# Kernel optimization log

Hardware: AMD Instinct MI355X
Metric: run time of the kernel (lower is better)

Reference implementation:

```python
import jax, jax.numpy as jnp
import numpy as np

B, S, H, E, D, K = 2, 4096, 1024, 8, 2048, 2


def setup_inputs() -> dict:
    key = jax.random.key(0)
    ks = jax.random.split(key, 6)
    scale = 0.02
    return {
        "x": jax.random.normal(ks[0], (B, S, H), dtype=jnp.float32),
        "gate_w": jax.random.normal(ks[1], (E, H), dtype=jnp.float32) * scale,
        "w1": jax.random.normal(ks[2], (E, H, D), dtype=jnp.float32) * scale,
        "b1": jnp.zeros((E, D), dtype=jnp.float32),
        "w2": jax.random.normal(ks[3], (E, D, H), dtype=jnp.float32) * scale,
        "b2": jnp.zeros((E, H), dtype=jnp.float32),
    }


def reference(x, gate_w, w1, b1, w2, b2):
    b, s, h = x.shape
    e = gate_w.shape[0]
    # Router
    router_logits = jnp.einsum('bsh,eh->bse', x, gate_w)
    router_probs = jax.nn.softmax(router_logits, axis=-1)
    top_k_probs, expert_idx = jax.lax.top_k(router_probs, K)      # [B,S,K]
    top_k_probs = top_k_probs / top_k_probs.sum(axis=-1, keepdims=True)
    # Aux load-balancing loss (faithful to source: mean over batch only -> [S,E])
    oh = jax.nn.one_hot(expert_idx, e, dtype=x.dtype)             # [B,S,K,E]
    tokens_per_expert = oh.sum(axis=-2).mean(axis=0)              # [S,E]
    avg_prob = router_probs.mean(axis=(0, 1))                     # [E]
    aux_loss = e * (tokens_per_expert * avg_prob).sum()
    # Dense combine weights per token per expert: [B*S, E]
    combine = (oh * top_k_probs[..., None]).sum(axis=-2).reshape(-1, e)
    # Expert MLPs, batched over experts (grouped GEMM form)
    xf = x.reshape(-1, h)                                         # [T,H]
    hid = jax.nn.gelu(jnp.einsum('th,ehd->etd', xf, w1) + b1[:, None, :],
                      approximate=False)                          # [E,T,D]
    y = jnp.einsum('etd,edh->eth', hid, w2) + b2[:, None, :]      # [E,T,H]
    out = jnp.einsum('te,eth->th', combine, y)                    # [T,H]
    return out.reshape(b, s, h), aux_loss
```

## Files before the change

kernel.cpp:

```cpp
#include <hip/hip_runtime.h>
#include <hip/hip_bf16.h>
#include <math.h>

#define Bdim 2
#define Sdim 4096
#define Hdim 1024
#define Edim 8
#define Ddim 2048
#define Tdim (Bdim*Sdim)

typedef __attribute__((ext_vector_type(8))) __bf16 bfv8;
typedef __attribute__((ext_vector_type(8))) short s16x8;
typedef __attribute__((ext_vector_type(4))) short s16x4;
typedef __attribute__((ext_vector_type(4))) float f32x4;

__device__ __forceinline__ short f2bf(float f) {
    union { float f; unsigned u; } a; a.f = f;
    unsigned r = (a.u + 0x7fffu + ((a.u >> 16) & 1u)) >> 16;
    return (short)r;
}
__device__ __forceinline__ float bf2f(short s) {
    union { unsigned u; float f; } a; a.u = ((unsigned)(unsigned short)s) << 16;
    return a.f;
}
__device__ __forceinline__ float fgelu(float x) {
    float u = fminf(x * (1.5957691f + 0.07135481f * x * x), 60.0f);
    float t = __expf(u);
    return x * t / (t + 1.0f);
}

typedef const __attribute__((address_space(1))) unsigned int ga_u32;
typedef __attribute__((address_space(3))) unsigned int la_u32;

__device__ __forceinline__ void gl_lds16(const void* g, void* l) {
    __builtin_amdgcn_global_load_lds((ga_u32*)g, (la_u32*)l, 16, 0, 0);
}

#define SYNC_PREF() do {                                   \
    asm volatile("s_waitcnt vmcnt(0)" ::: "memory");       \
    __builtin_amdgcn_s_barrier();                          \
    __builtin_amdgcn_sched_barrier(0);                     \
} while (0)

__global__ __launch_bounds__(256) void router_kernel(
    const float* __restrict__ x, const float* __restrict__ gw,
    int* __restrict__ cnt, float* __restrict__ psum,
    int* __restrict__ ltok, float* __restrict__ lw,
    short* __restrict__ xb)
{
    __shared__ float gws[Edim * Hdim];
    __shared__ int   lcnt[Edim], gbase[Edim];
    __shared__ int   s_e[32], s_pos[32], s_tok[32];
    __shared__ float s_w[32];
    __shared__ float s_ps[4][8];

    int tid = threadIdx.x;
    for (int i = tid; i < Edim * Hdim / 4; i += 256)
        ((float4*)gws)[i] = ((const float4*)gw)[i];
    if (tid < Edim) lcnt[tid] = 0;
    __syncthreads();

    int wave = tid >> 6, lane = tid & 63;
    float ps = 0.f;

    for (int i = 0; i < 4; ++i) {
        int t = blockIdx.x * 16 + wave * 4 + i;
        double acc[Edim];
#pragma unroll
        for (int e = 0; e < Edim; ++e) acc[e] = 0.0;
#pragma unroll
        for (int kq = 0; kq < 4; ++kq) {
            float4 xv = *(const float4*)(x + (size_t)t * Hdim + kq * 256 + lane * 4);
            if (xb) {
                s16x4 h; h[0]=f2bf(xv.x); h[1]=f2bf(xv.y); h[2]=f2bf(xv.z); h[3]=f2bf(xv.w);
                *(s16x4*)(xb + (size_t)t * Hdim + kq * 256 + lane * 4) = h;
            }
#pragma unroll
            for (int e = 0; e < Edim; ++e) {
                float4 wv = *(const float4*)(&gws[e * Hdim + kq * 256 + lane * 4]);
                acc[e] += (double)xv.x * wv.x + (double)xv.y * wv.y
                        + (double)xv.z * wv.z + (double)xv.w * wv.w;
            }
        }
#pragma unroll
        for (int e = 0; e < Edim; ++e) {
            acc[e] += __shfl_xor(acc[e], 1, 64);
            acc[e] += __shfl_xor(acc[e], 2, 64);
            acc[e] += __shfl_xor(acc[e], 4, 64);
        }
        int el = lane & 7;
        double v = acc[0];
#pragma unroll
        for (int e = 1; e < Edim; ++e) if (el == e) v = acc[e];
        v += __shfl_xor(v, 8, 64);
        v += __shfl_xor(v, 16, 64);
        v += __shfl_xor(v, 32, 64);
        double mx = v;
        mx = fmax(mx, __shfl_xor(mx, 1, 64));
        mx = fmax(mx, __shfl_xor(mx, 2, 64));
        mx = fmax(mx, __shfl_xor(mx, 4, 64));
        float ex = __expf((float)(v - mx));
        float sm = ex;
        sm += __shfl_xor(sm, 1, 64);
        sm += __shfl_xor(sm, 2, 64);
        sm += __shfl_xor(sm, 4, 64);
        ps += ex / sm;
        double le[8];
#pragma unroll
        for (int e = 0; e < 8; ++e) le[e] = __shfl(v, e, 8);
        if (lane == 0) {
            int e1 = 0;
#pragma unroll
            for (int e = 1; e < 8; ++e) if (le[e] > le[e1]) e1 = e;
            int e2 = -1;
#pragma unroll
            for (int e = 0; e < 8; ++e) {
                if (e == e1) continue;
                if (e2 < 0 || le[e] > le[e2]) e2 = e;
            }
            float r = __expf((float)(le[e2] - le[e1]));
            float w1v = 1.0f / (1.0f + r);
            int lt = (wave * 4 + i) * 2;
            int p1 = atomicAdd(&lcnt[e1], 1);
            s_e[lt] = e1; s_pos[lt] = p1; s_tok[lt] = 2*t;     s_w[lt] = w1v;
            int p2 = atomicAdd(&lcnt[e2], 1);
            s_e[lt+1] = e2; s_pos[lt+1] = p2; s_tok[lt+1] = 2*t+1; s_w[lt+1] = 1.0f - w1v;
        }
    }
    if (lane < 8) s_ps[wave][lane] = ps;
    __syncthreads();
    if (tid < 8) {
        atomicAdd(&psum[tid], s_ps[0][tid] + s_ps[1][tid] + s_ps[2][tid] + s_ps[3][tid]);
        gbase[tid] = atomicAdd(&cnt[tid], lcnt[tid]);
    }
    __syncthreads();
    if (tid < 32) {
        int e = s_e[tid];
        int pos = gbase[e] + s_pos[tid];
        ltok[e * Tdim + pos] = s_tok[tid];
        lw[e * Tdim + pos] = s_w[tid];
    }
}

__global__ void aux_kernel(const int* __restrict__ cnt,
                           const float* __restrict__ psum,
                           int* __restrict__ eoff,
                           float* __restrict__ out_aux)
{
    if (threadIdx.x == 0 && blockIdx.x == 0) {
        double s = 0.0;
        int run = 0;
        for (int e = 0; e < Edim; ++e) {
            eoff[e] = run;
            run += cnt[e];
            s += ((double)cnt[e] / (double)Bdim) * ((double)psum[e] / (double)Tdim);
        }
        out_aux[0] = (float)((double)Edim * s);
    }
}

__global__ __launch_bounds__(256) void convt_kernel(const float* __restrict__ w,
                                                    short* __restrict__ wt, int R, int C)
{
    int e = blockIdx.z;
    int r0 = blockIdx.y * 64, c0 = blockIdx.x * 64;
    __shared__ short t[64][76];
    int tid = threadIdx.x;
    {
        int r = tid >> 2, cs = (tid & 3) * 16;
        const float* src = w + ((size_t)e * R + r0 + r) * C + c0 + cs;
#pragma unroll
        for (int q = 0; q < 4; ++q) {
            float4 v = *(const float4*)(src + q * 4);
            s16x4 h; h[0]=f2bf(v.x); h[1]=f2bf(v.y); h[2]=f2bf(v.z); h[3]=f2bf(v.w);
            *(s16x4*)(&t[r][cs + q * 4]) = h;
        }
    }
    __syncthreads();
    {
        int c = tid >> 2, rs = (tid & 3) * 16;
        short tmp[16];
#pragma unroll
        for (int j = 0; j < 16; ++j) tmp[j] = t[rs + j][c];
        short* dst = wt + ((size_t)e * C + c0 + c) * R + r0 + rs;
        *(s16x8*)dst = *(s16x8*)tmp;
        *(s16x8*)(dst + 8) = *(s16x8*)(tmp + 8);
    }
}


__global__ __launch_bounds__(512, 2) void gemm1n_kernel(
    const short* __restrict__ xb, const short* __restrict__ w1t,
    const float* __restrict__ b1, const int* __restrict__ cnt,
    const int* __restrict__ eoff, const int* __restrict__ ltok,
    short* __restrict__ hid)
{
    constexpr int GXN = Ddim / 256;
    int id = blockIdx.x;
    int e = id & 7;
    unsigned rem = (unsigned)id >> 3;
    int bx = rem & (GXN - 1);
    int by = rem / GXN;

    int n_e = cnt[e];
    int row0 = by * 256;
    if (row0 >= n_e) return;
    int col0 = bx * 256;
    int slot0 = eoff[e];

    __shared__ short lds[65536];
    char* ldsb = (char*)lds;

    int tid = threadIdx.x;
    int w = tid >> 6, lane = tid & 63;

    const short* aSrc[4]; const short* bSrc[4];
    int dstOff[4];
#pragma unroll
    for (int i = 0; i < 4; ++i) {
        int chunk = w * 256 + i * 64 + lane;
        int row = chunk >> 3, q = chunk & 7;
        int sc = (q * 16) ^ ((row & 7) << 4);
        int gr = row0 + row; if (gr > n_e - 1) gr = n_e - 1;
        int tok = ltok[(size_t)e * Tdim + gr] >> 1;
        aSrc[i] = xb + (size_t)tok * Hdim + (sc >> 1);
        bSrc[i] = w1t + ((size_t)e * Ddim + col0 + row) * Hdim + (sc >> 1);
        dstOff[i] = chunk * 16;
    }

    int fr = lane & 15, kg = lane >> 4;
    int wm = (w >> 2) * 128, wn = (w & 3) * 64;
    int swz = (fr & 7) << 3;
    const short* pAk[2]; const short* pBk[2];
#pragma unroll
    for (int ks = 0; ks < 2; ++ks) {
        pAk[ks] = lds + (wm + fr) * 64 + ((ks * 32 + kg * 8) ^ swz);
        pBk[ks] = lds + 16384 + (wn + fr) * 64 + ((ks * 32 + kg * 8) ^ swz);
    }

    f32x4 acc[8][4];
#pragma unroll
    for (int m = 0; m < 8; ++m)
#pragma unroll
        for (int n = 0; n < 4; ++n) acc[m][n] = (f32x4)0.0f;

    auto stage = [&](int bufB) {
#pragma unroll
        for (int i = 0; i < 4; ++i) {
            gl_lds16(aSrc[i], ldsb + bufB + dstOff[i]);
            gl_lds16(bSrc[i], ldsb + bufB + 32768 + dstOff[i]);
            aSrc[i] += 64; bSrc[i] += 64;
        }
    };
    auto compute = [&](int bufS) {
#pragma unroll
        for (int ks = 0; ks < 2; ++ks) {
            bfv8 af[8], bf[4];
#pragma unroll
            for (int n = 0; n < 4; ++n) bf[n] = *(const bfv8*)(pBk[ks] + bufS + n * 1024);
#pragma unroll
            for (int m = 0; m < 8; ++m) af[m] = *(const bfv8*)(pAk[ks] + bufS + m * 1024);
#pragma unroll
            for (int m = 0; m < 8; ++m)
#pragma unroll
                for (int n = 0; n < 4; ++n)
                    acc[m][n] = __builtin_amdgcn_mfma_f32_16x16x32_bf16(af[m], bf[n], acc[m][n], 0, 0, 0);
        }
    };

    constexpr int NK = Hdim / 64;
    stage(0);
    SYNC_PREF();
    for (int k = 0; k < NK; k += 2) {
        stage(65536);
        compute(0);
        __builtin_amdgcn_sched_barrier(0);
        SYNC_PREF();
        if (k + 2 < NK) stage(0);
        compute(32768);
        __builtin_amdgcn_sched_barrier(0);
        SYNC_PREF();
    }

#pragma unroll
    for (int m = 0; m < 8; ++m) {
        int r0r = wm + m * 16 + kg * 4;
#pragma unroll
        for (int j = 0; j < 4; ++j) {
            int gr = row0 + r0r + j;
            if (gr >= n_e) continue;
            size_t hbase = (size_t)(slot0 + gr) * Ddim;
#pragma unroll
            for (int n = 0; n < 4; ++n) {
                int col = col0 + wn + n * 16 + fr;
                float v = acc[m][n][j] + b1[e * Ddim + col];
                hid[hbase + col] = f2bf(fgelu(v));
            }
        }
    }
}

__global__ __launch_bounds__(512, 2) void gemm2n_kernel(
    const short* __restrict__ hid, const short* __restrict__ w2t,
    const float* __restrict__ b2, const int* __restrict__ cnt,
    const int* __restrict__ eoff, const int* __restrict__ ltok,
    const float* __restrict__ lw, short* __restrict__ out2)
{
    constexpr int GXN = Hdim / 256;
    int id = blockIdx.x;
    int e = id & 7;
    unsigned rem = (unsigned)id >> 3;
    int bx = rem & (GXN - 1);
    int by = rem / GXN;

    int n_e = cnt[e];
    int row0 = by * 256;
    if (row0 >= n_e) return;
    int col0 = bx * 256;
    int slot0 = eoff[e];

    __shared__ short lds[65536];
    char* ldsb = (char*)lds;

    int tid = threadIdx.x;
    int w = tid >> 6, lane = tid & 63;

    const short* aSrc[4]; const short* bSrc[4];
    int dstOff[4];
#pragma unroll
    for (int i = 0; i < 4; ++i) {
        int chunk = w * 256 + i * 64 + lane;
        int row = chunk >> 3, q = chunk & 7;
        int sc = (q * 16) ^ ((row & 7) << 4);
        int gr = row0 + row; if (gr > n_e - 1) gr = n_e - 1;
        aSrc[i] = hid + (size_t)(slot0 + gr) * Ddim + (sc >> 1);
        bSrc[i] = w2t + ((size_t)e * Hdim + col0 + row) * Ddim + (sc >> 1);
        dstOff[i] = chunk * 16;
    }

    int fr = lane & 15, kg = lane >> 4;
    int wm = (w >> 2) * 128, wn = (w & 3) * 64;
    int swz = (fr & 7) << 3;
    const short* pAk[2]; const short* pBk[2];
#pragma unroll
    for (int ks = 0; ks < 2; ++ks) {
        pAk[ks] = lds + (wm + fr) * 64 + ((ks * 32 + kg * 8) ^ swz);
        pBk[ks] = lds + 16384 + (wn + fr) * 64 + ((ks * 32 + kg * 8) ^ swz);
    }

    f32x4 acc[8][4];
#pragma unroll
    for (int m = 0; m < 8; ++m)
#pragma unroll
        for (int n = 0; n < 4; ++n) acc[m][n] = (f32x4)0.0f;

    auto stage = [&](int bufB) {
#pragma unroll
        for (int i = 0; i < 4; ++i) {
            gl_lds16(aSrc[i], ldsb + bufB + dstOff[i]);
            gl_lds16(bSrc[i], ldsb + bufB + 32768 + dstOff[i]);
            aSrc[i] += 64; bSrc[i] += 64;
        }
    };
    auto compute = [&](int bufS) {
#pragma unroll
        for (int ks = 0; ks < 2; ++ks) {
            bfv8 af[8], bf[4];
#pragma unroll
            for (int n = 0; n < 4; ++n) bf[n] = *(const bfv8*)(pBk[ks] + bufS + n * 1024);
#pragma unroll
            for (int m = 0; m < 8; ++m) af[m] = *(const bfv8*)(pAk[ks] + bufS + m * 1024);
#pragma unroll
            for (int m = 0; m < 8; ++m)
#pragma unroll
                for (int n = 0; n < 4; ++n)
                    acc[m][n] = __builtin_amdgcn_mfma_f32_16x16x32_bf16(af[m], bf[n], acc[m][n], 0, 0, 0);
        }
    };

    constexpr int NK = Ddim / 64;
    stage(0);
    SYNC_PREF();
    for (int k = 0; k < NK; k += 2) {
        stage(65536);
        compute(0);
        __builtin_amdgcn_sched_barrier(0);
        SYNC_PREF();
        if (k + 2 < NK) stage(0);
        compute(32768);
        __builtin_amdgcn_sched_barrier(0);
        SYNC_PREF();
    }

#pragma unroll
    for (int m = 0; m < 8; ++m) {
        int r0r = wm + m * 16 + kg * 4;
#pragma unroll
        for (int j = 0; j < 4; ++j) {
            int gr = row0 + r0r + j;
            if (gr >= n_e) continue;
            int val = ltok[(size_t)e * Tdim + gr];
            float p = lw[(size_t)e * Tdim + gr];
            size_t obase = (size_t)val * Hdim;
#pragma unroll
            for (int n = 0; n < 4; ++n) {
                int col = col0 + wn + n * 16 + fr;
                float v = p * (acc[m][n][j] + b2[e * Hdim + col]);
                out2[obase + col] = f2bf(v);
            }
        }
    }
}

__global__ __launch_bounds__(256) void combine_kernel(const short* __restrict__ out2,
                                                      float* __restrict__ out)
{
    size_t i = ((size_t)blockIdx.x * 256 + threadIdx.x) * 8;
    size_t t = i >> 10;
    int h = (int)(i & 1023);
    s16x8 a = *(const s16x8*)(out2 + (t * 2) * 1024 + h);
    s16x8 b = *(const s16x8*)(out2 + (t * 2 + 1) * 1024 + h);
#pragma unroll
    for (int j = 0; j < 8; ++j)
        out[i + j] = bf2f(a[j]) + bf2f(b[j]);
}

#define FBK 64
#define FLDK 72

__global__ __launch_bounds__(256) void gemm1_fb(
    const float* __restrict__ x, const float* __restrict__ w1,
    const float* __restrict__ b1, const int* __restrict__ cnt,
    const int* __restrict__ ltok, short* __restrict__ hid,
    int CH, int row_base)
{
    int e = blockIdx.z;
    int n_e = cnt[e];
    int row0 = row_base + blockIdx.y * 128;
    if (row0 >= n_e) return;
    int col0 = blockIdx.x * 128;

    __shared__ short As[128][FLDK];
    __shared__ short Bs[128][FLDK];

    int tid = threadIdx.x;
    int arow = tid >> 1;
    int akh  = (tid & 1) * 32;
    int gr_a = row0 + arow;
    int tok = ltok[(size_t)e * Tdim + (gr_a < n_e ? gr_a : n_e - 1)] >> 1;
    const float* xrow = x + (size_t)tok * Hdim + akh;
    int bdg = (tid & 31) * 4;
    int bkg = (tid >> 5) * 4;

    int lane = tid & 63;
    int wid = tid >> 6;
    int wm = (wid >> 1) * 64, wn = (wid & 1) * 64;
    int fr = lane & 15, kg = lane >> 4;

    f32x4 acc[4][4];
#pragma unroll
    for (int m = 0; m < 4; ++m)
#pragma unroll
        for (int n = 0; n < 4; ++n) acc[m][n] = (f32x4)0.0f;

    const float* wB = w1 + (size_t)e * Hdim * Ddim + col0;

    for (int k0 = 0; k0 < Hdim; k0 += FBK) {
#pragma unroll
        for (int i = 0; i < 8; ++i) {
            float4 v = *(const float4*)(xrow + k0 + i * 4);
            s16x4 h; h[0] = f2bf(v.x); h[1] = f2bf(v.y); h[2] = f2bf(v.z); h[3] = f2bf(v.w);
            *(s16x4*)(&As[arow][akh + i * 4]) = h;
        }
#pragma unroll
        for (int r = 0; r < 2; ++r) {
            int kq = bkg + r * 32;
            float4 v0 = *(const float4*)(wB + (size_t)(k0 + kq + 0) * Ddim + bdg);
            float4 v1 = *(const float4*)(wB + (size_t)(k0 + kq + 1) * Ddim + bdg);
            float4 v2 = *(const float4*)(wB + (size_t)(k0 + kq + 2) * Ddim + bdg);
            float4 v3 = *(const float4*)(wB + (size_t)(k0 + kq + 3) * Ddim + bdg);
            const float* p0 = (const float*)&v0; const float* p1 = (const float*)&v1;
            const float* p2 = (const float*)&v2; const float* p3 = (const float*)&v3;
#pragma unroll
            for (int c = 0; c < 4; ++c) {
                s16x4 h; h[0] = f2bf(p0[c]); h[1] = f2bf(p1[c]); h[2] = f2bf(p2[c]); h[3] = f2bf(p3[c]);
                *(s16x4*)(&Bs[bdg + c][kq]) = h;
            }
        }
        __syncthreads();
        bfv8 af[4][2], bfr[4][2];
#pragma unroll
        for (int m = 0; m < 4; ++m)
#pragma unroll
            for (int kk = 0; kk < 2; ++kk)
                af[m][kk] = *(const bfv8*)(&As[wm + m * 16 + fr][kk * 32 + kg * 8]);
#pragma unroll
        for (int n = 0; n < 4; ++n)
#pragma unroll
            for (int kk = 0; kk < 2; ++kk)
                bfr[n][kk] = *(const bfv8*)(&Bs[wn + n * 16 + fr][kk * 32 + kg * 8]);
#pragma unroll
        for (int m = 0; m < 4; ++m)
#pragma unroll
            for (int n = 0; n < 4; ++n) {
                acc[m][n] = __builtin_amdgcn_mfma_f32_16x16x32_bf16(af[m][0], bfr[n][0], acc[m][n], 0, 0, 0);
                acc[m][n] = __builtin_amdgcn_mfma_f32_16x16x32_bf16(af[m][1], bfr[n][1], acc[m][n], 0, 0, 0);
            }
        __syncthreads();
    }

    int lr0 = row0 - row_base;
#pragma unroll
    for (int m = 0; m < 4; ++m) {
        int r0r = wm + m * 16 + kg * 4;
#pragma unroll
        for (int j = 0; j < 4; ++j) {
            int gr = row0 + r0r + j;
            if (gr >= n_e) continue;
            size_t hbase = ((size_t)e * CH + (size_t)(lr0 + r0r + j)) * Ddim;
#pragma unroll
            for (int n = 0; n < 4; ++n) {
                int col = col0 + wn + n * 16 + fr;
                float v = acc[m][n][j] + b1[e * Ddim + col];
                float g = 0.5f * v * (1.0f + erff(v * 0.70710678118654752440f));
                hid[hbase + col] = f2bf(g);
            }
        }
    }
}

__global__ __launch_bounds__(256) void gemm2_fb(
    const short* __restrict__ hid, const float* __restrict__ w2,
    const float* __restrict__ b2, const int* __restrict__ cnt,
    const int* __restrict__ ltok, const float* __restrict__ lw,
    float* __restrict__ out, int CH, int row_base)
{
    int e = blockIdx.z;
    int n_e = cnt[e];
    int row0 = row_base + blockIdx.y * 128;
    if (row0 >= n_e) return;
    int col0 = blockIdx.x * 128;

    __shared__ short As[128][FLDK];
    __shared__ short Bs[128][FLDK];

    int tid = threadIdx.x;
    int arow = tid >> 1;
    int akh  = (tid & 1) * 32;
    const short* hrow = hid + ((size_t)e * CH + (size_t)(row0 - row_base + arow)) * Ddim + akh;
    int bdg = (tid & 31) * 4;
    int bkg = (tid >> 5) * 4;

    int lane = tid & 63;
    int wid = tid >> 6;
    int wm = (wid >> 1) * 64, wn = (wid & 1) * 64;
    int fr = lane & 15, kg = lane >> 4;

    f32x4 acc[4][4];
#pragma unroll
    for (int m = 0; m < 4; ++m)
#pragma unroll
        for (int n = 0; n < 4; ++n) acc[m][n] = (f32x4)0.0f;

    const float* wB = w2 + (size_t)e * Ddim * Hdim + col0;

    for (int k0 = 0; k0 < Ddim; k0 += FBK) {
#pragma unroll
        for (int i = 0; i < 4; ++i) {
            s16x8 v = *(const s16x8*)(hrow + k0 + i * 8);
            *(s16x8*)(&As[arow][akh + i * 8]) = v;
        }
#pragma unroll
        for (int r = 0; r < 2; ++r) {
            int kq = bkg + r * 32;
            float4 v0 = *(const float4*)(wB + (size_t)(k0 + kq + 0) * Hdim + bdg);
            float4 v1 = *(const float4*)(wB + (size_t)(k0 + kq + 1) * Hdim + bdg);
            float4 v2 = *(const float4*)(wB + (size_t)(k0 + kq + 2) * Hdim + bdg);
            float4 v3 = *(const float4*)(wB + (size_t)(k0 + kq + 3) * Hdim + bdg);
            const float* p0 = (const float*)&v0; const float* p1 = (const float*)&v1;
            const float* p2 = (const float*)&v2; const float* p3 = (const float*)&v3;
#pragma unroll
            for (int c = 0; c < 4; ++c) {
                s16x4 h; h[0] = f2bf(p0[c]); h[1] = f2bf(p1[c]); h[2] = f2bf(p2[c]); h[3] = f2bf(p3[c]);
                *(s16x4*)(&Bs[bdg + c][kq]) = h;
            }
        }
        __syncthreads();
        bfv8 af[4][2], bfr[4][2];
#pragma unroll
        for (int m = 0; m < 4; ++m)
#pragma unroll
            for (int kk = 0; kk < 2; ++kk)
                af[m][kk] = *(const bfv8*)(&As[wm + m * 16 + fr][kk * 32 + kg * 8]);
#pragma unroll
        for (int n = 0; n < 4; ++n)
#pragma unroll
            for (int kk = 0; kk < 2; ++kk)
                bfr[n][kk] = *(const bfv8*)(&Bs[wn + n * 16 + fr][kk * 32 + kg * 8]);
#pragma unroll
        for (int m = 0; m < 4; ++m)
#pragma unroll
            for (int n = 0; n < 4; ++n) {
                acc[m][n] = __builtin_amdgcn_mfma_f32_16x16x32_bf16(af[m][0], bfr[n][0], acc[m][n], 0, 0, 0);
                acc[m][n] = __builtin_amdgcn_mfma_f32_16x16x32_bf16(af[m][1], bfr[n][1], acc[m][n], 0, 0, 0);
            }
        __syncthreads();
    }

#pragma unroll
    for (int m = 0; m < 4; ++m) {
        int r0r = wm + m * 16 + kg * 4;
#pragma unroll
        for (int j = 0; j < 4; ++j) {
            int gr = row0 + r0r + j;
            if (gr >= n_e) continue;
            int tok = ltok[(size_t)e * Tdim + gr] >> 1;
            float p = lw[(size_t)e * Tdim + gr];
#pragma unroll
            for (int n = 0; n < 4; ++n) {
                int col = col0 + wn + n * 16 + fr;
                float v = p * (acc[m][n][j] + b2[e * Hdim + col]);
                atomicAdd(&out[(size_t)tok * Hdim + col], v);
            }
        }
    }
}

extern "C" void kernel_launch(void* const* d_in, const int* in_sizes, int n_in,
                              void* d_out, int out_size, void* d_ws, size_t ws_size,
                              hipStream_t stream)
{
    const float* x  = (const float*)d_in[0];
    const float* gw = (const float*)d_in[1];
    const float* w1 = (const float*)d_in[2];
    const float* b1 = (const float*)d_in[3];
    const float* w2 = (const float*)d_in[4];
    const float* b2 = (const float*)d_in[5];
    float* out = (float*)d_out;

    char* wsb = (char*)d_ws;
    int*   cnt  = (int*)wsb;
    float* psum = (float*)(wsb + 32);
    int*   eoff = (int*)(wsb + 64);
    int*   ltok = (int*)(wsb + 128);
    float* lwp  = (float*)(wsb + 128 + (size_t)Edim * Tdim * 4);
    size_t lists_end = 128 + (size_t)Edim * Tdim * 8;

    size_t xb_sz = (size_t)Tdim * Hdim * 2;
    size_t w1t_sz = (size_t)Edim * Hdim * Ddim * 2;
    size_t w2t_sz = w1t_sz;
    size_t hid_sz = (size_t)(2 * Tdim) * Ddim * 2;
    size_t req = lists_end + xb_sz + w1t_sz + w2t_sz + hid_sz;

    hipMemsetAsync(wsb, 0, 128, stream);

    if (req <= ws_size) {
        short* xb   = (short*)(wsb + lists_end);
        short* w1t  = (short*)(wsb + lists_end + xb_sz);
        short* w2t  = (short*)(wsb + lists_end + xb_sz + w1t_sz);
        short* hid  = (short*)(wsb + lists_end + xb_sz + w1t_sz + w2t_sz);
        short* out2 = w1t;

        convt_kernel<<<dim3(Ddim / 64, Hdim / 64, Edim), 256, 0, stream>>>(w1, w1t, Hdim, Ddim);
        convt_kernel<<<dim3(Hdim / 64, Ddim / 64, Edim), 256, 0, stream>>>(w2, w2t, Ddim, Hdim);
        router_kernel<<<Tdim / 16, 256, 0, stream>>>(x, gw, cnt, psum, ltok, lwp, xb);
        aux_kernel<<<1, 64, 0, stream>>>(cnt, psum, eoff, out + (size_t)Tdim * Hdim);

        gemm1n_kernel<<<(Ddim / 256) * 32 * Edim, 512, 0, stream>>>(
            xb, w1t, b1, cnt, eoff, ltok, hid);
        gemm2n_kernel<<<(Hdim / 256) * 32 * Edim, 512, 0, stream>>>(
            hid, w2t, b2, cnt, eoff, ltok, lwp, out2);
        combine_kernel<<<(size_t)Tdim * Hdim / 2048, 256, 0, stream>>>(out2, out);
    } else {
        short* hid = (short*)(wsb + lists_end);
        int CH2 = 2048;
        while (CH2 > 128 && lists_end + (size_t)Edim * CH2 * Ddim * 2 > ws_size) CH2 >>= 1;

        hipMemsetAsync(d_out, 0, (size_t)out_size * 4, stream);
        router_kernel<<<Tdim / 16, 256, 0, stream>>>(x, gw, cnt, psum, ltok, lwp, nullptr);
        aux_kernel<<<1, 64, 0, stream>>>(cnt, psum, eoff, out + (size_t)Tdim * Hdim);

        int chunks = Tdim / CH2;
        for (int c = 0; c < chunks; ++c) {
            gemm1_fb<<<dim3(Ddim / 128, CH2 / 128, Edim), 256, 0, stream>>>(
                x, w1, b1, cnt, ltok, hid, CH2, c * CH2);
            gemm2_fb<<<dim3(Hdim / 128, CH2 / 128, Edim), 256, 0, stream>>>(
                hid, w2, b2, cnt, ltok, lwp, out, CH2, c * CH2);
        }
    }
}
```

Baseline: 340.1 us.

## Split K-tiles into half stages with partial vmcnt waits in expert GEMMs

New measurement: 337.7 us. Within noise of the previous version (-0.7%).

```diff
diff --git a/kernel.cpp b/kernel.cpp
--- a/kernel.cpp
+++ b/kernel.cpp
@@ -36,10 +36,10 @@
     __builtin_amdgcn_global_load_lds((ga_u32*)g, (la_u32*)l, 16, 0, 0);
 }
 
-#define SYNC_PREF() do {                                   \
-    asm volatile("s_waitcnt vmcnt(0)" ::: "memory");       \
-    __builtin_amdgcn_s_barrier();                          \
-    __builtin_amdgcn_sched_barrier(0);                     \
+#define WAIT_BAR(N) do {                                     \
+    asm volatile("s_waitcnt vmcnt(" #N ")" ::: "memory");    \
+    __builtin_amdgcn_s_barrier();                            \
+    __builtin_amdgcn_sched_barrier(0);                       \
 } while (0)
 
 __global__ __launch_bounds__(256) void router_kernel(
@@ -214,28 +214,34 @@
     int tid = threadIdx.x;
     int w = tid >> 6, lane = tid & 63;
 
-    const short* aSrc[4]; const short* bSrc[4];
-    int dstOff[4];
-#pragma unroll
-    for (int i = 0; i < 4; ++i) {
-        int chunk = w * 256 + i * 64 + lane;
-        int row = chunk >> 3, q = chunk & 7;
-        int sc = (q * 16) ^ ((row & 7) << 4);
+    const short* aS[2]; const short* bS[2];
+    int oA[2];
+#pragma unroll
+    for (int j = 0; j < 2; ++j) {
+        int o = tid * 16 + j * 8192;
+        oA[j] = o;
+        int eff = o ^ (((o >> 7) & 7) << 4);
+        int row = ((eff >> 7) << 1) | ((eff >> 6) & 1);
+        int kB  = eff & 63;
         int gr = row0 + row; if (gr > n_e - 1) gr = n_e - 1;
         int tok = ltok[(size_t)e * Tdim + gr] >> 1;
-        aSrc[i] = xb + (size_t)tok * Hdim + (sc >> 1);
-        bSrc[i] = w1t + ((size_t)e * Ddim + col0 + row) * Hdim + (sc >> 1);
-        dstOff[i] = chunk * 16;
+        aS[j] = xb + (size_t)tok * Hdim + (kB >> 1);
+        bS[j] = w1t + ((size_t)e * Ddim + col0 + row) * Hdim + (kB >> 1);
     }
 
     int fr = lane & 15, kg = lane >> 4;
     int wm = (w >> 2) * 128, wn = (w & 3) * 64;
-    int swz = (fr & 7) << 3;
-    const short* pAk[2]; const short* pBk[2];
-#pragma unroll
-    for (int ks = 0; ks < 2; ++ks) {
-        pAk[ks] = lds + (wm + fr) * 64 + ((ks * 32 + kg * 8) ^ swz);
-        pBk[ks] = lds + 16384 + (wn + fr) * 64 + ((ks * 32 + kg * 8) ^ swz);
+
+    int offA[8], offB[4];
+#pragma unroll
+    for (int m = 0; m < 8; ++m) {
+        int r = wm + m * 16 + fr;
+        offA[m] = (r >> 1) * 64 + ((((r & 1) * 32) + kg * 8) ^ (((r >> 1) & 7) << 3));
+    }
+#pragma unroll
+    for (int n = 0; n < 4; ++n) {
+        int r = wn + n * 16 + fr;
+        offB[n] = (r >> 1) * 64 + ((((r & 1) * 32) + kg * 8) ^ (((r >> 1) & 7) << 3));
     }
 
     f32x4 acc[8][4];
@@ -244,43 +250,42 @@
 #pragma unroll
         for (int n = 0; n < 4; ++n) acc[m][n] = (f32x4)0.0f;
 
-    auto stage = [&](int bufB) {
-#pragma unroll
-        for (int i = 0; i < 4; ++i) {
-            gl_lds16(aSrc[i], ldsb + bufB + dstOff[i]);
-            gl_lds16(bSrc[i], ldsb + bufB + 32768 + dstOff[i]);
-            aSrc[i] += 64; bSrc[i] += 64;
+    auto stage = [&](int dstB) {
+#pragma unroll
+        for (int j = 0; j < 2; ++j) {
+            gl_lds16(aS[j], ldsb + dstB + oA[j]);
+            gl_lds16(bS[j], ldsb + dstB + 32768 + oA[j]);
+            aS[j] += 32; bS[j] += 32;
         }
     };
-    auto compute = [&](int bufS) {
-#pragma unroll
-        for (int ks = 0; ks < 2; ++ks) {
-            bfv8 af[8], bf[4];
-#pragma unroll
-            for (int n = 0; n < 4; ++n) bf[n] = *(const bfv8*)(pBk[ks] + bufS + n * 1024);
-#pragma unroll
-            for (int m = 0; m < 8; ++m) af[m] = *(const bfv8*)(pAk[ks] + bufS + m * 1024);
-#pragma unroll
-            for (int m = 0; m < 8; ++m)
-#pragma unroll
-                for (int n = 0; n < 4; ++n)
-                    acc[m][n] = __builtin_amdgcn_mfma_f32_16x16x32_bf16(af[m], bf[n], acc[m][n], 0, 0, 0);
-        }
+    auto computeH = [&](int baseSh) {
+        bfv8 af[8], bf[4];
+#pragma unroll
+        for (int n = 0; n < 4; ++n) bf[n] = *(const bfv8*)(lds + baseSh + 16384 + offB[n]);
+#pragma unroll
+        for (int m = 0; m < 8; ++m) af[m] = *(const bfv8*)(lds + baseSh + offA[m]);
+        __builtin_amdgcn_s_setprio(1);
+#pragma unroll
+        for (int m = 0; m < 8; ++m)
+#pragma unroll
+            for (int n = 0; n < 4; ++n)
+                acc[m][n] = __builtin_amdgcn_mfma_f32_16x16x32_bf16(af[m], bf[n], acc[m][n], 0, 0, 0);
+        __builtin_amdgcn_s_setprio(0);
     };
 
     constexpr int NK = Hdim / 64;
     stage(0);
-    SYNC_PREF();
-    for (int k = 0; k < NK; k += 2) {
-        stage(65536);
-        compute(0);
-        __builtin_amdgcn_sched_barrier(0);
-        SYNC_PREF();
-        if (k + 2 < NK) stage(0);
-        compute(32768);
-        __builtin_amdgcn_sched_barrier(0);
-        SYNC_PREF();
-    }
+    stage(16384);
+    for (int k = 0; k < NK - 2; k += 2) {
+        stage(65536);         WAIT_BAR(8); computeH(0);
+        stage(65536 + 16384); WAIT_BAR(8); computeH(8192);
+        stage(0);             WAIT_BAR(8); computeH(32768);
+        stage(16384);         WAIT_BAR(8); computeH(40960);
+    }
+    stage(65536);         WAIT_BAR(8); computeH(0);
+    stage(65536 + 16384); WAIT_BAR(8); computeH(8192);
+    WAIT_BAR(4); computeH(32768);
+    WAIT_BAR(0); computeH(40960);
 
 #pragma unroll
     for (int m = 0; m < 8; ++m) {
@@ -325,27 +330,33 @@
     int tid = threadIdx.x;
     int w = tid >> 6, lane = tid & 63;
 
-    const short* aSrc[4]; const short* bSrc[4];
-    int dstOff[4];
-#pragma unroll
-    for (int i = 0; i < 4; ++i) {
-        int chunk = w * 256 + i * 64 + lane;
-        int row = chunk >> 3, q = chunk & 7;
-        int sc = (q * 16) ^ ((row & 7) << 4);
+    const short* aS[2]; const short* bS[2];
+    int oA[2];
+#pragma unroll
+    for (int j = 0; j < 2; ++j) {
+        int o = tid * 16 + j * 8192;
+        oA[j] = o;
+        int eff = o ^ (((o >> 7) & 7) << 4);
+        int row = ((eff >> 7) << 1) | ((eff >> 6) & 1);
+        int kB  = eff & 63;
         int gr = row0 + row; if (gr > n_e - 1) gr = n_e - 1;
-        aSrc[i] = hid + (size_t)(slot0 + gr) * Ddim + (sc >> 1);
-        bSrc[i] = w2t + ((size_t)e * Hdim + col0 + row) * Ddim + (sc >> 1);
-        dstOff[i] = chunk * 16;
+        aS[j] = hid + (size_t)(slot0 + gr) * Ddim + (kB >> 1);
+        bS[j] = w2t + ((size_t)e * Hdim + col0 + row) * Ddim + (kB >> 1);
     }
 
     int fr = lane & 15, kg = lane >> 4;
     int wm = (w >> 2) * 128, wn = (w & 3) * 64;
-    int swz = (fr & 7) << 3;
-    const short* pAk[2]; const short* pBk[2];
-#pragma unroll
-    for (int ks = 0; ks < 2; ++ks) {
-        pAk[ks] = lds + (wm + fr) * 64 + ((ks * 32 + kg * 8) ^ swz);
-        pBk[ks] = lds + 16384 + (wn + fr) * 64 + ((ks * 32 + kg * 8) ^ swz);
+
+    int offA[8], offB[4];
+#pragma unroll
+    for (int m = 0; m < 8; ++m) {
+        int r = wm + m * 16 + fr;
+        offA[m] = (r >> 1) * 64 + ((((r & 1) * 32) + kg * 8) ^ (((r >> 1) & 7) << 3));
+    }
+#pragma unroll
+    for (int n = 0; n < 4; ++n) {
+        int r = wn + n * 16 + fr;
+        offB[n] = (r >> 1) * 64 + ((((r & 1) * 32) + kg * 8) ^ (((r >> 1) & 7) << 3));
     }
 
     f32x4 acc[8][4];
@@ -354,43 +365,42 @@
 #pragma unroll
         for (int n = 0; n < 4; ++n) acc[m][n] = (f32x4)0.0f;
 
-    auto stage = [&](int bufB) {
-#pragma unroll
-        for (int i = 0; i < 4; ++i) {
-            gl_lds16(aSrc[i], ldsb + bufB + dstOff[i]);
-            gl_lds16(bSrc[i], ldsb + bufB + 32768 + dstOff[i]);
-            aSrc[i] += 64; bSrc[i] += 64;
+    auto stage = [&](int dstB) {
+#pragma unroll
+        for (int j = 0; j < 2; ++j) {
+            gl_lds16(aS[j], ldsb + dstB + oA[j]);
+            gl_lds16(bS[j], ldsb + dstB + 32768 + oA[j]);
+            aS[j] += 32; bS[j] += 32;
         }
     };
-    auto compute = [&](int bufS) {
-#pragma unroll
-        for (int ks = 0; ks < 2; ++ks) {
-            bfv8 af[8], bf[4];
-#pragma unroll
-            for (int n = 0; n < 4; ++n) bf[n] = *(const bfv8*)(pBk[ks] + bufS + n * 1024);
-#pragma unroll
-            for (int m = 0; m < 8; ++m) af[m] = *(const bfv8*)(pAk[ks] + bufS + m * 1024);
-#pragma unroll
-            for (int m = 0; m < 8; ++m)
-#pragma unroll
-                for (int n = 0; n < 4; ++n)
-                    acc[m][n] = __builtin_amdgcn_mfma_f32_16x16x32_bf16(af[m], bf[n], acc[m][n], 0, 0, 0);
-        }
+    auto computeH = [&](int baseSh) {
+        bfv8 af[8], bf[4];
+#pragma unroll
+        for (int n = 0; n < 4; ++n) bf[n] = *(const bfv8*)(lds + baseSh + 16384 + offB[n]);
+#pragma unroll
+        for (int m = 0; m < 8; ++m) af[m] = *(const bfv8*)(lds + baseSh + offA[m]);
+        __builtin_amdgcn_s_setprio(1);
+#pragma unroll
+        for (int m = 0; m < 8; ++m)
+#pragma unroll
+            for (int n = 0; n < 4; ++n)
+                acc[m][n] = __builtin_amdgcn_mfma_f32_16x16x32_bf16(af[m], bf[n], acc[m][n], 0, 0, 0);
+        __builtin_amdgcn_s_setprio(0);
     };
 
     constexpr int NK = Ddim / 64;
     stage(0);
-    SYNC_PREF();
-    for (int k = 0; k < NK; k += 2) {
-        stage(65536);
-        compute(0);
-        __builtin_amdgcn_sched_barrier(0);
-        SYNC_PREF();
-        if (k + 2 < NK) stage(0);
-        compute(32768);
-        __builtin_amdgcn_sched_barrier(0);
-        SYNC_PREF();
-    }
+    stage(16384);
+    for (int k = 0; k < NK - 2; k += 2) {
+        stage(65536);         WAIT_BAR(8); computeH(0);
+        stage(65536 + 16384); WAIT_BAR(8); computeH(8192);
+        stage(0);             WAIT_BAR(8); computeH(32768);
+        stage(16384);         WAIT_BAR(8); computeH(40960);
+    }
+    stage(65536);         WAIT_BAR(8); computeH(0);
+    stage(65536 + 16384); WAIT_BAR(8); computeH(8192);
+    WAIT_BAR(4); computeH(32768);
+    WAIT_BAR(0); computeH(40960);
 
 #pragma unroll
     for (int m = 0; m < 8; ++m) {
```
